# Performance work log

Hardware: AMD Instinct MI355X
Metric: run time of the kernel (lower is better)

## Reference

```python
import jax, jax.numpy as jnp
import numpy as np

N, E, H = 6144, 64, 8
D = E * H  # 512
EPS = 1e-5


def _layernorm(v, g, b):
    m = jnp.mean(v, axis=-1, keepdims=True)
    var = jnp.mean((v - m) ** 2, axis=-1, keepdims=True)
    return (v - m) * jax.lax.rsqrt(var + EPS) * g + b


def setup_inputs() -> dict:
    key = jax.random.key(0)
    ks = jax.random.split(key, 4)
    x = jax.random.normal(ks[0], (N, E), dtype=jnp.float32)
    batch = jnp.sort(jax.random.randint(ks[1], (N,), 0, 256)).astype(jnp.int64)
    W_qkv = jax.random.normal(ks[2], (E, 3 * D), dtype=jnp.float32) * (1.0 / np.sqrt(E))
    b_qkv = jnp.zeros((3 * D,), dtype=jnp.float32)
    W_out = jax.random.normal(ks[3], (D, E), dtype=jnp.float32) * (1.0 / np.sqrt(D))
    b_out = jnp.zeros((E,), dtype=jnp.float32)
    return {
        "x": x, "batch": batch,
        "ln1_g": jnp.ones((E,), jnp.float32), "ln1_b": jnp.zeros((E,), jnp.float32),
        "W_qkv": W_qkv, "b_qkv": b_qkv,
        "ln2_g": jnp.ones((D,), jnp.float32), "ln2_b": jnp.zeros((D,), jnp.float32),
        "W_out": W_out, "b_out": b_out,
    }


def reference(x, batch, ln1_g, ln1_b, W_qkv, b_qkv, ln2_g, ln2_b, W_out, b_out):
    n = x.shape[0]
    h1 = _layernorm(x, ln1_g, ln1_b)                       # [N, E]
    kqv = h1 @ W_qkv + b_qkv                               # [N, 3D]
    K, Q, V = jnp.split(kqv, 3, axis=-1)                   # each [N, D], order K,Q,V per torch split
    # 'n (h d) -> h n d' with per-head dim d = E
    Q = Q.reshape(n, H, E).transpose(1, 0, 2)
    K = K.reshape(n, H, E).transpose(1, 0, 2)
    V = V.reshape(n, H, E).transpose(1, 0, 2)
    scores = jnp.einsum('hnd,hmd->hnm', Q, K) / np.sqrt(D)  # NOTE: scale by sqrt(D)=sqrt(H*E), as in source
    mask = batch[None, :, None] == batch[None, None, :]     # block-diagonal per-graph mask
    scores = jnp.where(mask, scores, -jnp.inf)
    attn = jax.nn.softmax(scores, axis=-1)                  # [H, N, N]
    out = jnp.einsum('hnm,hmd->hnd', attn, V)               # [H, N, E]
    out = out.transpose(1, 0, 2).reshape(n, D)              # 'h n d -> n (h d)'
    y = _layernorm(out, ln2_g, ln2_b) @ W_out + b_out       # out_proj with use_norm_layer=True
    return y
```

## Files before the change

kernel.cpp:

```cpp
#include <hip/hip_runtime.h>
#include <math.h>

#define N 6144
#define E 64
#define H 8
#define D 512
#define TD 1536
#define EPS 1e-5f
#define SCALE 0.04419417382415922f
#define RMAX 64

typedef __attribute__((ext_vector_type(8))) short bf16x8;
typedef __attribute__((ext_vector_type(4))) float f32x4;

static __device__ __forceinline__ unsigned short f2bf(float f) {
    union { float f; unsigned int u; } v; v.f = f;
    unsigned int r = v.u + 0x7FFFu + ((v.u >> 16) & 1u);
    return (unsigned short)(r >> 16);
}
static __device__ __forceinline__ float bf2f(unsigned short u) {
    union { unsigned int u; float f; } v; v.u = ((unsigned int)u) << 16;
    return v.f;
}

__global__ __launch_bounds__(256) void prep_kernel(
    const float* __restrict__ x, const float* __restrict__ ln1g,
    const float* __restrict__ ln1b, const float* __restrict__ W_qkv,
    const float* __restrict__ W_out, const int* __restrict__ batch,
    unsigned short* __restrict__ Wt, unsigned short* __restrict__ Wot,
    int* __restrict__ bound, unsigned short* __restrict__ h1g)
{
    const int t = threadIdx.x, lane = t & 63, wv = t >> 6;
    if (blockIdx.x < 32) {
        const int tid = blockIdx.x * 256 + t;
        if (tid < N) {
            const int bv = batch[tid];
            const int prev = tid ? batch[tid - 1] : -1;
            if (bv != prev)
                for (int v = prev + 1; v <= bv; ++v) bound[v] = tid;
            if (tid == N - 1)
                for (int v = bv + 1; v <= 256; ++v) bound[v] = N;
        }
        for (int i = tid; i < 64 * TD; i += 8192) {
            const int k = i / TD, j = i - k * TD;
            Wt[j * 64 + k] = f2bf(W_qkv[i]);
        }
        for (int i = tid; i < 512 * 64; i += 8192) {
            const int k = i >> 6, j = i & 63;
            Wot[j * 512 + k] = f2bf(W_out[i]);
        }
    } else {
        const int row = (blockIdx.x - 32) * 4 + wv;
        const float v = x[(size_t)row * E + lane];
        float sm = v, sq = v * v;
        #pragma unroll
        for (int off = 1; off < 64; off <<= 1) {
            sm += __shfl_xor(sm, off);
            sq += __shfl_xor(sq, off);
        }
        const float mean = sm * (1.f / 64.f);
        const float var  = sq * (1.f / 64.f) - mean * mean;
        h1g[(size_t)row * 64 + lane] =
            f2bf((v - mean) * rsqrtf(var + EPS) * ln1g[lane] + ln1b[lane]);
    }
}

__global__ __launch_bounds__(256) void seghead_kernel(
    const unsigned short* __restrict__ h1g, const unsigned short* __restrict__ Wt,
    const float* __restrict__ b_qkv, const int* __restrict__ bound,
    unsigned short* __restrict__ attb)
{
    __shared__ unsigned short Qs[RMAX][72];
    __shared__ unsigned short Ks[RMAX][72];
    __shared__ unsigned short Vs[64][72];
    __shared__ unsigned short Ps[RMAX][72];

    const int t = threadIdx.x, lane = t & 63, wv = t >> 6;
    const int lr = lane & 15, lg = lane >> 4;
    const int b = blockIdx.x, h = blockIdx.y;

    const int s = bound[b];
    const int e = bound[b + 1];

    const int ct = wv;
    const int jK = h * 64 + ct * 16;
    const int jQ = 512 + jK;
    const int jV = 1024 + jK;
    const bf16x8 wK0 = *(const bf16x8*)&Wt[(size_t)(jK + lr) * 64 + lg * 8];
    const bf16x8 wK1 = *(const bf16x8*)&Wt[(size_t)(jK + lr) * 64 + 32 + lg * 8];
    const bf16x8 wQ0 = *(const bf16x8*)&Wt[(size_t)(jQ + lr) * 64 + lg * 8];
    const bf16x8 wQ1 = *(const bf16x8*)&Wt[(size_t)(jQ + lr) * 64 + 32 + lg * 8];
    const bf16x8 wV0 = *(const bf16x8*)&Wt[(size_t)(jV + lr) * 64 + lg * 8];
    const bf16x8 wV1 = *(const bf16x8*)&Wt[(size_t)(jV + lr) * 64 + 32 + lg * 8];
    const float bK = b_qkv[jK + lr];
    const float bQ = b_qkv[jQ + lr];
    const float bV = b_qkv[jV + lr];

    int R = e - s;
    if (R <= 0) return;
    if (R > RMAX) R = RMAX;
    const int NT = (R + 15) >> 4;
    const int RT = NT * 16;
    const int KB = (RT + 31) >> 5;

    if (RT < KB * 32) {
        for (int idx = t; idx < 64 * 16; idx += 256) {
            const int dd = idx >> 4, cc = RT + (idx & 15);
            if (cc < KB * 32) Vs[dd][cc] = 0;
        }
    }

    #pragma unroll
    for (int rt = 0; rt < 4; ++rt) {
        if (rt < NT) {
            int row = s + rt * 16 + lr;
            row = row < N ? row : N - 1;
            const bf16x8 a0 = *(const bf16x8*)&h1g[(size_t)row * 64 + lg * 8];
            const bf16x8 a1 = *(const bf16x8*)&h1g[(size_t)row * 64 + 32 + lg * 8];
            f32x4 dK = {0,0,0,0}, dQ = {0,0,0,0}, dV = {0,0,0,0};
            dK = __builtin_amdgcn_mfma_f32_16x16x32_bf16(a0, wK0, dK, 0, 0, 0);
            dK = __builtin_amdgcn_mfma_f32_16x16x32_bf16(a1, wK1, dK, 0, 0, 0);
            dQ = __builtin_amdgcn_mfma_f32_16x16x32_bf16(a0, wQ0, dQ, 0, 0, 0);
            dQ = __builtin_amdgcn_mfma_f32_16x16x32_bf16(a1, wQ1, dQ, 0, 0, 0);
            dV = __builtin_amdgcn_mfma_f32_16x16x32_bf16(a0, wV0, dV, 0, 0, 0);
            dV = __builtin_amdgcn_mfma_f32_16x16x32_bf16(a1, wV1, dV, 0, 0, 0);
            const int n4 = rt * 16 + lg * 4;
            #pragma unroll
            for (int r = 0; r < 4; ++r) {
                Ks[n4 + r][ct * 16 + lr] = f2bf(dK[r] + bK);
                Qs[n4 + r][ct * 16 + lr] = f2bf(dQ[r] + bQ);
            }
            union { unsigned short us[4]; uint2 u2; } pk;
            #pragma unroll
            for (int r = 0; r < 4; ++r) pk.us[r] = f2bf(dV[r] + bV);
            *(uint2*)&Vs[ct * 16 + lr][n4] = pk.u2;
        }
    }
    __syncthreads();

    bf16x8 ones;
    #pragma unroll
    for (int j = 0; j < 8; ++j) ones[j] = (short)0x3F80;

    for (int qt = wv; qt < NT; qt += 4) {
        const bf16x8 qf0 = *(const bf16x8*)&Qs[qt * 16 + lr][lg * 8];
        const bf16x8 qf1 = *(const bf16x8*)&Qs[qt * 16 + lr][32 + lg * 8];
        for (int kt = 0; kt < 2 * KB; ++kt) {
            if (kt < NT) {
                const bf16x8 kf0 = *(const bf16x8*)&Ks[kt * 16 + lr][lg * 8];
                const bf16x8 kf1 = *(const bf16x8*)&Ks[kt * 16 + lr][32 + lg * 8];
                f32x4 dsc = {0.f, 0.f, 0.f, 0.f};
                dsc = __builtin_amdgcn_mfma_f32_16x16x32_bf16(qf0, kf0, dsc, 0, 0, 0);
                dsc = __builtin_amdgcn_mfma_f32_16x16x32_bf16(qf1, kf1, dsc, 0, 0, 0);
                const bool valid = (kt * 16 + lr) < R;
                #pragma unroll
                for (int r = 0; r < 4; ++r)
                    Ps[qt * 16 + lg * 4 + r][kt * 16 + lr] =
                        valid ? f2bf(__expf(dsc[r] * SCALE)) : 0;
            } else {
                #pragma unroll
                for (int r = 0; r < 4; ++r)
                    Ps[qt * 16 + lg * 4 + r][kt * 16 + lr] = 0;
            }
        }
        asm volatile("s_waitcnt lgkmcnt(0)" ::: "memory");

        f32x4 o0 = {0,0,0,0}, o1 = {0,0,0,0}, o2 = {0,0,0,0}, o3 = {0,0,0,0};
        f32x4 sac = {0,0,0,0};
        for (int kb = 0; kb < KB; ++kb) {
            const bf16x8 pa = *(const bf16x8*)&Ps[qt * 16 + lr][kb * 32 + lg * 8];
            sac = __builtin_amdgcn_mfma_f32_16x16x32_bf16(pa, ones, sac, 0, 0, 0);
            const bf16x8 v0 = *(const bf16x8*)&Vs[lr][kb * 32 + lg * 8];
            const bf16x8 v1 = *(const bf16x8*)&Vs[16 + lr][kb * 32 + lg * 8];
            const bf16x8 v2 = *(const bf16x8*)&Vs[32 + lr][kb * 32 + lg * 8];
            const bf16x8 v3 = *(const bf16x8*)&Vs[48 + lr][kb * 32 + lg * 8];
            o0 = __builtin_amdgcn_mfma_f32_16x16x32_bf16(pa, v0, o0, 0, 0, 0);
            o1 = __builtin_amdgcn_mfma_f32_16x16x32_bf16(pa, v1, o1, 0, 0, 0);
            o2 = __builtin_amdgcn_mfma_f32_16x16x32_bf16(pa, v2, o2, 0, 0, 0);
            o3 = __builtin_amdgcn_mfma_f32_16x16x32_bf16(pa, v3, o3, 0, 0, 0);
        }

        #pragma unroll
        for (int r = 0; r < 4; ++r) {
            const float inv = 1.f / sac[r];
            const int q = qt * 16 + lg * 4 + r;
            Ps[q][lr]      = f2bf(o0[r] * inv);
            Ps[q][16 + lr] = f2bf(o1[r] * inv);
            Ps[q][32 + lr] = f2bf(o2[r] * inv);
            Ps[q][48 + lr] = f2bf(o3[r] * inv);
        }
        asm volatile("s_waitcnt lgkmcnt(0)" ::: "memory");
        #pragma unroll
        for (int pass = 0; pass < 2; ++pass) {
            const int qi = pass * 8 + (lane >> 3);
            const int q  = qt * 16 + qi;
            const int dd = (lane & 7) * 8;
            if (q < R)
                *(bf16x8*)(attb + (size_t)(s + q) * D + h * 64 + dd) =
                    *(const bf16x8*)&Ps[q][dd];
        }
    }
}

__global__ __launch_bounds__(256) void ln2_out_kernel(
    const unsigned short* __restrict__ att, const float* __restrict__ g,
    const float* __restrict__ b, const unsigned short* __restrict__ Wot,
    const float* __restrict__ bias, float* __restrict__ y)
{
    __shared__ unsigned short h2[16][520];
    const int t = threadIdx.x, lane = t & 63, wv = t >> 6;
    const int row0 = blockIdx.x * 16;
    const int lr = lane & 15, lg = lane >> 4;

    const float4 ga = *(const float4*)&g[lane * 8];
    const float4 gb = *(const float4*)&g[lane * 8 + 4];
    const float4 ba = *(const float4*)&b[lane * 8];
    const float4 bb = *(const float4*)&b[lane * 8 + 4];
    const float gv[8] = {ga.x, ga.y, ga.z, ga.w, gb.x, gb.y, gb.z, gb.w};
    const float bv[8] = {ba.x, ba.y, ba.z, ba.w, bb.x, bb.y, bb.z, bb.w};

    #pragma unroll
    for (int i = 0; i < 4; ++i) {
        const int r = wv * 4 + i;
        const bf16x8 v8 = *(const bf16x8*)(att + (size_t)(row0 + r) * D + lane * 8);
        float vals[8];
        float sm = 0.f, sq = 0.f;
        #pragma unroll
        for (int c = 0; c < 8; ++c) {
            vals[c] = bf2f((unsigned short)v8[c]);
            sm += vals[c];
            sq += vals[c] * vals[c];
        }
        #pragma unroll
        for (int off = 1; off < 64; off <<= 1) {
            sm += __shfl_xor(sm, off);
            sq += __shfl_xor(sq, off);
        }
        const float mean = sm * (1.f / 512.f);
        const float var  = sq * (1.f / 512.f) - mean * mean;
        const float rstd = rsqrtf(var + EPS);
        bf16x8 hv;
        #pragma unroll
        for (int c = 0; c < 8; ++c)
            hv[c] = (short)f2bf((vals[c] - mean) * rstd * gv[c] + bv[c]);
        *(bf16x8*)&h2[r][lane * 8] = hv;
    }
    __syncthreads();

    const int j0 = wv * 16;
    f32x4 acc = {0.f, 0.f, 0.f, 0.f};
    #pragma unroll
    for (int ks = 0; ks < 16; ++ks) {
        const bf16x8 a  = *(const bf16x8*)&h2[lr][ks * 32 + lg * 8];
        const bf16x8 wb = *(const bf16x8*)&Wot[(size_t)(j0 + lr) * D + ks * 32 + lg * 8];
        acc = __builtin_amdgcn_mfma_f32_16x16x32_bf16(a, wb, acc, 0, 0, 0);
    }
    const float bj = bias[j0 + lr];
    #pragma unroll
    for (int r = 0; r < 4; ++r)
        y[(size_t)(row0 + lg * 4 + r) * 64 + j0 + lr] = acc[r] + bj;
}

extern "C" void kernel_launch(void* const* d_in, const int* in_sizes, int n_in,
                              void* d_out, int out_size, void* d_ws, size_t ws_size,
                              hipStream_t stream) {
    const float* x     = (const float*)d_in[0];
    const int*   batch = (const int*)  d_in[1];
    const float* ln1_g = (const float*)d_in[2];
    const float* ln1_b = (const float*)d_in[3];
    const float* W_qkv = (const float*)d_in[4];
    const float* b_qkv = (const float*)d_in[5];
    const float* ln2_g = (const float*)d_in[6];
    const float* ln2_b = (const float*)d_in[7];
    const float* W_out = (const float*)d_in[8];
    const float* b_out = (const float*)d_in[9];
    float* y = (float*)d_out;

    unsigned short* Wt   = (unsigned short*)d_ws;
    unsigned short* Wot  = Wt  + (size_t)TD * 64;
    unsigned short* h1g  = Wot + (size_t)64 * D;
    unsigned short* attb = h1g + (size_t)N * 64;
    int* bound = (int*)(attb + (size_t)N * D);

    hipLaunchKernelGGL(prep_kernel, dim3(1568), dim3(256), 0, stream,
                       x, ln1_g, ln1_b, W_qkv, W_out, batch, Wt, Wot, bound, h1g);
    hipLaunchKernelGGL(seghead_kernel, dim3(256, 8), dim3(256), 0, stream,
                       h1g, Wt, b_qkv, bound, attb);
    hipLaunchKernelGGL(ln2_out_kernel, dim3(N / 16), dim3(256), 0, stream,
                       attb, ln2_g, ln2_b, Wot, b_out, y);
}
```

Baseline: 34.23 us.

## Split attention work into finer per-wave tiles across query and key tiles

Work in the attention kernel used to be split by query tile only, so each wave ran a whole query tile. It is now split into two phases separated by a block barrier. The first phase spreads (query tile, key tile) score blocks across all waves. The second phase spreads (query tile, output half) PV blocks across waves and writes normalized outputs into the Q buffer before storing. The aim is better load balance among the four waves when a graph has few query tiles, at the cost of an extra __syncthreads, Q fragments reloaded per score block, and the softmax row sum computed twice.

After: 33.90 us. Within noise of the previous version (-1.0%).

```diff
diff --git a/kernel.cpp b/kernel.cpp
--- a/kernel.cpp
+++ b/kernel.cpp
@@ -142,63 +142,57 @@
     #pragma unroll
     for (int j = 0; j < 8; ++j) ones[j] = (short)0x3F80;
 
-    for (int qt = wv; qt < NT; qt += 4) {
-        const bf16x8 qf0 = *(const bf16x8*)&Qs[qt * 16 + lr][lg * 8];
-        const bf16x8 qf1 = *(const bf16x8*)&Qs[qt * 16 + lr][32 + lg * 8];
-        for (int kt = 0; kt < 2 * KB; ++kt) {
-            if (kt < NT) {
-                const bf16x8 kf0 = *(const bf16x8*)&Ks[kt * 16 + lr][lg * 8];
-                const bf16x8 kf1 = *(const bf16x8*)&Ks[kt * 16 + lr][32 + lg * 8];
-                f32x4 dsc = {0.f, 0.f, 0.f, 0.f};
-                dsc = __builtin_amdgcn_mfma_f32_16x16x32_bf16(qf0, kf0, dsc, 0, 0, 0);
-                dsc = __builtin_amdgcn_mfma_f32_16x16x32_bf16(qf1, kf1, dsc, 0, 0, 0);
-                const bool valid = (kt * 16 + lr) < R;
-                #pragma unroll
-                for (int r = 0; r < 4; ++r)
-                    Ps[qt * 16 + lg * 4 + r][kt * 16 + lr] =
-                        valid ? f2bf(__expf(dsc[r] * SCALE)) : 0;
-            } else {
-                #pragma unroll
-                for (int r = 0; r < 4; ++r)
-                    Ps[qt * 16 + lg * 4 + r][kt * 16 + lr] = 0;
-            }
-        }
-        asm volatile("s_waitcnt lgkmcnt(0)" ::: "memory");
-
-        f32x4 o0 = {0,0,0,0}, o1 = {0,0,0,0}, o2 = {0,0,0,0}, o3 = {0,0,0,0};
-        f32x4 sac = {0,0,0,0};
+    const int KT2 = 2 * KB;
+    const int ksh = KB;
+
+    for (int c = wv; c < NT * KT2; c += 4) {
+        const int qt = c >> ksh, kt = c & (KT2 - 1);
+        if (kt < NT) {
+            const bf16x8 qf0 = *(const bf16x8*)&Qs[qt * 16 + lr][lg * 8];
+            const bf16x8 qf1 = *(const bf16x8*)&Qs[qt * 16 + lr][32 + lg * 8];
+            const bf16x8 kf0 = *(const bf16x8*)&Ks[kt * 16 + lr][lg * 8];
+            const bf16x8 kf1 = *(const bf16x8*)&Ks[kt * 16 + lr][32 + lg * 8];
+            f32x4 dsc = {0.f, 0.f, 0.f, 0.f};
+            dsc = __builtin_amdgcn_mfma_f32_16x16x32_bf16(qf0, kf0, dsc, 0, 0, 0);
+            dsc = __builtin_amdgcn_mfma_f32_16x16x32_bf16(qf1, kf1, dsc, 0, 0, 0);
+            const bool valid = (kt * 16 + lr) < R;
+            #pragma unroll
+            for (int r = 0; r < 4; ++r)
+                Ps[qt * 16 + lg * 4 + r][kt * 16 + lr] =
+                    valid ? f2bf(__expf(dsc[r] * SCALE)) : 0;
+        } else {
+            #pragma unroll
+            for (int r = 0; r < 4; ++r)
+                Ps[qt * 16 + lg * 4 + r][kt * 16 + lr] = 0;
+        }
+    }
+    __syncthreads();
+
+    for (int c = wv; c < NT * 2; c += 4) {
+        const int qt = c >> 1, half = c & 1;
+        f32x4 oA = {0,0,0,0}, oB = {0,0,0,0}, sac = {0,0,0,0};
         for (int kb = 0; kb < KB; ++kb) {
             const bf16x8 pa = *(const bf16x8*)&Ps[qt * 16 + lr][kb * 32 + lg * 8];
             sac = __builtin_amdgcn_mfma_f32_16x16x32_bf16(pa, ones, sac, 0, 0, 0);
-            const bf16x8 v0 = *(const bf16x8*)&Vs[lr][kb * 32 + lg * 8];
-            const bf16x8 v1 = *(const bf16x8*)&Vs[16 + lr][kb * 32 + lg * 8];
-            const bf16x8 v2 = *(const bf16x8*)&Vs[32 + lr][kb * 32 + lg * 8];
-            const bf16x8 v3 = *(const bf16x8*)&Vs[48 + lr][kb * 32 + lg * 8];
-            o0 = __builtin_amdgcn_mfma_f32_16x16x32_bf16(pa, v0, o0, 0, 0, 0);
-            o1 = __builtin_amdgcn_mfma_f32_16x16x32_bf16(pa, v1, o1, 0, 0, 0);
-            o2 = __builtin_amdgcn_mfma_f32_16x16x32_bf16(pa, v2, o2, 0, 0, 0);
-            o3 = __builtin_amdgcn_mfma_f32_16x16x32_bf16(pa, v3, o3, 0, 0, 0);
-        }
-
+            const bf16x8 vA = *(const bf16x8*)&Vs[half * 32 + lr][kb * 32 + lg * 8];
+            const bf16x8 vB = *(const bf16x8*)&Vs[half * 32 + 16 + lr][kb * 32 + lg * 8];
+            oA = __builtin_amdgcn_mfma_f32_16x16x32_bf16(pa, vA, oA, 0, 0, 0);
+            oB = __builtin_amdgcn_mfma_f32_16x16x32_bf16(pa, vB, oB, 0, 0, 0);
+        }
         #pragma unroll
         for (int r = 0; r < 4; ++r) {
             const float inv = 1.f / sac[r];
             const int q = qt * 16 + lg * 4 + r;
-            Ps[q][lr]      = f2bf(o0[r] * inv);
-            Ps[q][16 + lr] = f2bf(o1[r] * inv);
-            Ps[q][32 + lr] = f2bf(o2[r] * inv);
-            Ps[q][48 + lr] = f2bf(o3[r] * inv);
+            Qs[q][half * 32 + lr]      = f2bf(oA[r] * inv);
+            Qs[q][half * 32 + 16 + lr] = f2bf(oB[r] * inv);
         }
         asm volatile("s_waitcnt lgkmcnt(0)" ::: "memory");
-        #pragma unroll
-        for (int pass = 0; pass < 2; ++pass) {
-            const int qi = pass * 8 + (lane >> 3);
-            const int q  = qt * 16 + qi;
-            const int dd = (lane & 7) * 8;
-            if (q < R)
-                *(bf16x8*)(attb + (size_t)(s + q) * D + h * 64 + dd) =
-                    *(const bf16x8*)&Ps[q][dd];
-        }
+        const int qi = lane >> 2;
+        const int q  = qt * 16 + qi;
+        const int dd = half * 32 + (lane & 3) * 8;
+        if (q < R)
+            *(bf16x8*)(attb + (size_t)(s + q) * D + h * 64 + dd) =
+                *(const bf16x8*)&Qs[q][dd];
     }
 }
 
```
